# Performance work log

Measured on AMD Instinct MI355X. Metric: run time of the kernel, lower is better.

Reference implementation:

```python
import jax, jax.numpy as jnp
import numpy as np

B, D, H = 16384, 64, 256

def setup_inputs() -> dict:
    key = jax.random.key(0)
    ks = jax.random.split(key, 24)
    s = 0.05
    inp = {
        'x':   jax.random.normal(ks[0], (B, D), dtype=jnp.float32),
        # stacked per-feature MLPs (torch ModuleList of Linear(1,H)->ReLU->Linear(H,H)->ReLU->Linear(H,1))
        'W1':  jax.random.normal(ks[1], (D, H), dtype=jnp.float32) * s,      # in=1
        'b1':  jax.random.normal(ks[2], (D, H), dtype=jnp.float32) * s,
        'W2':  jax.random.normal(ks[3], (D, H, H), dtype=jnp.float32) * s,
        'b2':  jax.random.normal(ks[4], (D, H), dtype=jnp.float32) * s,
        'W3':  jax.random.normal(ks[5], (D, H), dtype=jnp.float32) * s,      # out=1
        'b3':  jax.random.normal(ks[6], (D,), dtype=jnp.float32) * s,
        # attention fusion
        'Wq':  jax.random.normal(ks[7], (H, D), dtype=jnp.float32) * s,
        'bq':  jax.random.normal(ks[8], (H,), dtype=jnp.float32) * s,
        'Wk':  jax.random.normal(ks[9], (H, D), dtype=jnp.float32) * s,
        'bk':  jax.random.normal(ks[10], (H,), dtype=jnp.float32) * s,
        'Ws':  jax.random.normal(ks[11], (D, H), dtype=jnp.float32) * s,
        'bs':  jax.random.normal(ks[12], (D,), dtype=jnp.float32) * s,
        # cross MLP: Linear(D,H)->ReLU->Linear(H,1)
        'Wc1': jax.random.normal(ks[13], (H, D), dtype=jnp.float32) * s,
        'bc1': jax.random.normal(ks[14], (H,), dtype=jnp.float32) * s,
        'Wc2': jax.random.normal(ks[15], (H,), dtype=jnp.float32) * s,
        'bc2': jax.random.normal(ks[16], (1,), dtype=jnp.float32) * s,
        # g_func: Linear(1,H)->ReLU->Linear(H,1)
        'Wg1': jax.random.normal(ks[17], (H,), dtype=jnp.float32) * s,
        'bg1': jax.random.normal(ks[18], (H,), dtype=jnp.float32) * s,
        'Wg2': jax.random.normal(ks[19], (H,), dtype=jnp.float32) * s,
        'bg2': jax.random.normal(ks[20], (1,), dtype=jnp.float32) * s,
    }
    return inp

def reference(x, W1, b1, W2, b2, W3, b3, Wq, bq, Wk, bk, Ws, bs,
              Wc1, bc1, Wc2, bc2, Wg1, bg1, Wg2, bg2):
    # per-feature 3-layer MLPs, vectorized over the feature axis d
    a1 = jax.nn.relu(x[:, :, None] * W1[None] + b1[None])           # [B, D, H]
    a2 = jax.nn.relu(jnp.einsum('bdh,dhk->bdk', a1, W2) + b2[None]) # [B, D, H]
    h_cat = jnp.einsum('bdh,dh->bd', a2, W3) + b3[None]             # [B, D]
    # tiny tanh-softmax attention fusion
    q = h_cat @ Wq.T + bq                                           # [B, H]
    k = h_cat @ Wk.T + bk                                           # [B, H]
    scores = jnp.tanh(q * k) @ Ws.T + bs                            # [B, D]
    wts = jax.nn.softmax(scores, axis=1)
    weighted = jnp.sum(h_cat * wts, axis=1, keepdims=True)          # [B, 1]
    cross = jax.nn.relu(h_cat @ Wc1.T + bc1) @ Wc2[:, None] + bc2   # [B, 1]
    comb = weighted + cross                                         # [B, 1]
    out = jax.nn.relu(comb * Wg1[None] + bg1[None]) @ Wg2[:, None] + bg2  # [B, 1]
    return out
```

## Files before the change

kernel.cpp:

```cpp
#include <hip/hip_runtime.h>
#include <stdint.h>

#define Bn 16384
#define Dn 64
#define Hn 256

typedef short bf16x8 __attribute__((ext_vector_type(8)));
typedef float f32x4 __attribute__((ext_vector_type(4)));
typedef float f32x16 __attribute__((ext_vector_type(16)));

__device__ __forceinline__ unsigned f2bf1(float f) {
  unsigned u = __float_as_uint(f);
  return (u + 0x7FFFu + ((u >> 16) & 1u)) >> 16;
}

__global__ __launch_bounds__(256) void pack_w2(const float* __restrict__ W2,
                                               unsigned short* __restrict__ Bp) {
  int gidx = blockIdx.x * 4 + (threadIdx.x >> 6);
  int lane = threadIdx.x & 63;
  int d  = gidx >> 7;
  int s  = (gidx >> 3) & 15;
  int nb = gidx & 7;
  int k0 = s * 16 + ((lane >> 5) << 3);
  int n  = (nb << 5) + (lane & 31);
  const float* src = W2 + ((size_t)d * Hn + k0) * Hn + n;
  unsigned t[8];
  #pragma unroll
  for (int b = 0; b < 8; ++b) t[b] = f2bf1(src[(size_t)b * Hn]);
  uint4 w;
  w.x = t[0] | (t[1] << 16);
  w.y = t[2] | (t[3] << 16);
  w.z = t[4] | (t[5] << 16);
  w.w = t[6] | (t[7] << 16);
  size_t off = (((size_t)gidx) * 64 + lane) * 8;
  *(uint4*)(Bp + off) = w;
}

__global__ __launch_bounds__(256) void prep_t(
    const float* __restrict__ Wq, const float* __restrict__ Wk,
    const float* __restrict__ Wc1, const float* __restrict__ Ws,
    float* __restrict__ WqT, float* __restrict__ WkT,
    float* __restrict__ Wc1T, float* __restrict__ WsT) {
  int t = blockIdx.x * 256 + threadIdx.x;
  int h = t >> 6, dd = t & 63;
  WqT[dd * 256 + h]  = Wq[h * 64 + dd];
  WkT[dd * 256 + h]  = Wk[h * 64 + dd];
  Wc1T[dd * 256 + h] = Wc1[h * 64 + dd];
  WsT[h * 64 + dd]   = Ws[dd * 256 + h];
}

__global__ __launch_bounds__(768, 1) void gemm_hcat(
    const float* __restrict__ x, const float* __restrict__ W1,
    const float* __restrict__ b1, const float* __restrict__ b2,
    const float* __restrict__ W3, const float* __restrict__ b3,
    const unsigned short* __restrict__ Bp, float* __restrict__ hcT) {
  __shared__ char Bs[131072];

  int bid = blockIdx.x;
  int xcd = bid & 7;
  int dl = (bid >> 3) & 7;
  int chunk = bid >> 6;
  int d = xcd * 8 + dl;
  int base = chunk * 4096;

  int tid = threadIdx.x;
  int lane = tid & 63;
  int w = tid >> 6;
  int l31 = lane & 31;
  int hsel = lane >> 5;

  const unsigned short* BpD = Bp + (size_t)d * 65536;
  const float* W1d = W1 + d * Hn;
  const float* b1d = b1 + d * Hn;
  const float* b2d = b2 + d * Hn;
  const float* W3d = W3 + d * Hn;
  float b3d = b3[d];

  #pragma unroll
  for (int i = 0; i < 11; ++i) {
    int idx = i * 768 + tid;
    if (idx < 8192) {
      const void* g = (const void*)(BpD + (size_t)idx * 8);
      void* l = (void*)(Bs + (size_t)idx * 16);
      __builtin_amdgcn_global_load_lds((const __attribute__((address_space(1))) void*)g,
                                       (__attribute__((address_space(3))) void*)l, 16, 0, 0);
    }
  }
  __syncthreads();

  for (int t = w; t < 128; t += 12) {
    int row = base + t * 32 + l31;
    float xv = x[(size_t)row * Dn + d];

    bf16x8 af[16];
    #pragma unroll
    for (int s = 0; s < 16; ++s) {
      int k = s * 16 + (hsel << 3);
      float4 wa = *(const float4*)(W1d + k);
      float4 wb = *(const float4*)(W1d + k + 4);
      float4 ba = *(const float4*)(b1d + k);
      float4 bb = *(const float4*)(b1d + k + 4);
      float v0 = fmaxf(fmaf(xv, wa.x, ba.x), 0.f);
      float v1 = fmaxf(fmaf(xv, wa.y, ba.y), 0.f);
      float v2 = fmaxf(fmaf(xv, wa.z, ba.z), 0.f);
      float v3 = fmaxf(fmaf(xv, wa.w, ba.w), 0.f);
      float v4 = fmaxf(fmaf(xv, wb.x, bb.x), 0.f);
      float v5 = fmaxf(fmaf(xv, wb.y, bb.y), 0.f);
      float v6 = fmaxf(fmaf(xv, wb.z, bb.z), 0.f);
      float v7 = fmaxf(fmaf(xv, wb.w, bb.w), 0.f);
      union { uint4 u; bf16x8 v; } pk;
      asm("v_cvt_pk_bf16_f32 %0, %1, %2" : "=v"(pk.u.x) : "v"(v0), "v"(v1));
      asm("v_cvt_pk_bf16_f32 %0, %1, %2" : "=v"(pk.u.y) : "v"(v2), "v"(v3));
      asm("v_cvt_pk_bf16_f32 %0, %1, %2" : "=v"(pk.u.z) : "v"(v4), "v"(v5));
      asm("v_cvt_pk_bf16_f32 %0, %1, %2" : "=v"(pk.u.w) : "v"(v6), "v"(v7));
      af[s] = pk.v;
    }

    float ph = 0.f;
    #pragma unroll 1
    for (int nb = 0; nb < 8; ++nb) {
      int cb = (nb << 5) + (hsel << 2);

      f32x16 acc;
      #pragma unroll
      for (int q = 0; q < 4; ++q) {
        float4 bv = *(const float4*)(b2d + cb + (q << 3));
        acc[4 * q + 0] = bv.x;
        acc[4 * q + 1] = bv.y;
        acc[4 * q + 2] = bv.z;
        acc[4 * q + 3] = bv.w;
      }

      __builtin_amdgcn_s_setprio(1);
      #pragma unroll
      for (int s = 0; s < 16; ++s) {
        bf16x8 bfr = *(const bf16x8*)(Bs + ((((s << 3) + nb) << 6) + lane) * 16);
        acc = __builtin_amdgcn_mfma_f32_32x32x16_bf16(bfr, af[s], acc, 0, 0, 0);
      }
      __builtin_amdgcn_s_setprio(0);

      #pragma unroll
      for (int q = 0; q < 4; ++q) {
        float4 wv = *(const float4*)(W3d + cb + (q << 3));
        ph = fmaf(fmaxf(acc[4 * q + 0], 0.f), wv.x, ph);
        ph = fmaf(fmaxf(acc[4 * q + 1], 0.f), wv.y, ph);
        ph = fmaf(fmaxf(acc[4 * q + 2], 0.f), wv.z, ph);
        ph = fmaf(fmaxf(acc[4 * q + 3], 0.f), wv.w, ph);
      }
    }

    ph += __shfl_xor(ph, 32);
    if (lane < 32) hcT[(size_t)d * Bn + row] = ph + b3d;
  }
}

__global__ __launch_bounds__(256) void fused_tail(
    const float* __restrict__ hcT, const float* __restrict__ WqT,
    const float* __restrict__ bq, const float* __restrict__ WkT,
    const float* __restrict__ bk, const float* __restrict__ WsT,
    const float* __restrict__ bs, const float* __restrict__ Wc1T,
    const float* __restrict__ bc1, const float* __restrict__ Wc2,
    const float* __restrict__ bc2, const float* __restrict__ Wg1,
    const float* __restrict__ bg1, const float* __restrict__ Wg2,
    const float* __restrict__ bg2, float* __restrict__ out) {
  __shared__ float hcs[4][4][64];
  __shared__ float ts[4][4][256];
  int wid = threadIdx.x >> 6;
  int lane = threadIdx.x & 63;
  int r0 = (blockIdx.x * 4 + wid) * 4;
  float4 hc4 = *(const float4*)(hcT + (size_t)lane * Bn + r0);
  hcs[wid][0][lane] = hc4.x;
  hcs[wid][1][lane] = hc4.y;
  hcs[wid][2][lane] = hc4.z;
  hcs[wid][3][lane] = hc4.w;
  __syncthreads();

  float qv[4][4], kv[4][4], cv[4][4];
  #pragma unroll
  for (int j = 0; j < 4; ++j) {
    int h = lane + 64 * j;
    float bqv = bq[h], bkv = bk[h], bcv = bc1[h];
    #pragma unroll
    for (int r = 0; r < 4; ++r) { qv[r][j] = bqv; kv[r][j] = bkv; cv[r][j] = bcv; }
  }
  for (int d2 = 0; d2 < 64; ++d2) {
    float hv0 = hcs[wid][0][d2], hv1 = hcs[wid][1][d2];
    float hv2 = hcs[wid][2][d2], hv3 = hcs[wid][3][d2];
    #pragma unroll
    for (int j = 0; j < 4; ++j) {
      int h = lane + 64 * j;
      float wq = WqT[d2 * 256 + h], wk = WkT[d2 * 256 + h], wc = Wc1T[d2 * 256 + h];
      qv[0][j] = fmaf(wq, hv0, qv[0][j]); qv[1][j] = fmaf(wq, hv1, qv[1][j]);
      qv[2][j] = fmaf(wq, hv2, qv[2][j]); qv[3][j] = fmaf(wq, hv3, qv[3][j]);
      kv[0][j] = fmaf(wk, hv0, kv[0][j]); kv[1][j] = fmaf(wk, hv1, kv[1][j]);
      kv[2][j] = fmaf(wk, hv2, kv[2][j]); kv[3][j] = fmaf(wk, hv3, kv[3][j]);
      cv[0][j] = fmaf(wc, hv0, cv[0][j]); cv[1][j] = fmaf(wc, hv1, cv[1][j]);
      cv[2][j] = fmaf(wc, hv2, cv[2][j]); cv[3][j] = fmaf(wc, hv3, cv[3][j]);
    }
  }
  #pragma unroll
  for (int r = 0; r < 4; ++r)
    #pragma unroll
    for (int j = 0; j < 4; ++j)
      ts[wid][r][lane + 64 * j] = tanhf(qv[r][j] * kv[r][j]);
  __syncthreads();

  float sc[4];
  { float b = bs[lane]; sc[0] = b; sc[1] = b; sc[2] = b; sc[3] = b; }
  for (int h2 = 0; h2 < 256; ++h2) {
    float w = WsT[h2 * 64 + lane];
    sc[0] = fmaf(w, ts[wid][0][h2], sc[0]);
    sc[1] = fmaf(w, ts[wid][1][h2], sc[1]);
    sc[2] = fmaf(w, ts[wid][2][h2], sc[2]);
    sc[3] = fmaf(w, ts[wid][3][h2], sc[3]);
  }

  float hcr[4] = {hc4.x, hc4.y, hc4.z, hc4.w};
  float res[4];
  #pragma unroll
  for (int r = 0; r < 4; ++r) {
    float s = sc[r];
    float mx = s;
    #pragma unroll
    for (int off = 1; off < 64; off <<= 1) mx = fmaxf(mx, __shfl_xor(mx, off));
    float e = __expf(s - mx);
    float se = e;
    #pragma unroll
    for (int off = 1; off < 64; off <<= 1) se += __shfl_xor(se, off);
    float wgt = hcr[r] * (e / se);
    #pragma unroll
    for (int off = 1; off < 64; off <<= 1) wgt += __shfl_xor(wgt, off);
    float cp = 0.f;
    #pragma unroll
    for (int j = 0; j < 4; ++j) cp = fmaf(fmaxf(cv[r][j], 0.f), Wc2[lane + 64 * j], cp);
    #pragma unroll
    for (int off = 1; off < 64; off <<= 1) cp += __shfl_xor(cp, off);
    float comb = wgt + cp + bc2[0];
    float fp = 0.f;
    #pragma unroll
    for (int j = 0; j < 4; ++j) {
      int h = lane + 64 * j;
      fp = fmaf(fmaxf(fmaf(comb, Wg1[h], bg1[h]), 0.f), Wg2[h], fp);
    }
    #pragma unroll
    for (int off = 1; off < 64; off <<= 1) fp += __shfl_xor(fp, off);
    res[r] = fp + bg2[0];
  }
  if (lane == 0) {
    float4 o = make_float4(res[0], res[1], res[2], res[3]);
    *(float4*)(out + r0) = o;
  }
}

extern "C" void kernel_launch(void* const* d_in, const int* in_sizes, int n_in,
                              void* d_out, int out_size, void* d_ws, size_t ws_size,
                              hipStream_t stream) {
  const float* x   = (const float*)d_in[0];
  const float* W1  = (const float*)d_in[1];
  const float* b1  = (const float*)d_in[2];
  const float* W2  = (const float*)d_in[3];
  const float* b2  = (const float*)d_in[4];
  const float* W3  = (const float*)d_in[5];
  const float* b3  = (const float*)d_in[6];
  const float* Wq  = (const float*)d_in[7];
  const float* bq  = (const float*)d_in[8];
  const float* Wk  = (const float*)d_in[9];
  const float* bk  = (const float*)d_in[10];
  const float* Ws  = (const float*)d_in[11];
  const float* bs  = (const float*)d_in[12];
  const float* Wc1 = (const float*)d_in[13];
  const float* bc1 = (const float*)d_in[14];
  const float* Wc2 = (const float*)d_in[15];
  const float* bc2 = (const float*)d_in[16];
  const float* Wg1 = (const float*)d_in[17];
  const float* bg1 = (const float*)d_in[18];
  const float* Wg2 = (const float*)d_in[19];
  const float* bg2 = (const float*)d_in[20];

  unsigned short* Bp = (unsigned short*)d_ws;
  float* hcT  = (float*)((char*)d_ws + 8388608);
  float* WqT  = (float*)((char*)d_ws + 12582912);
  float* WkT  = WqT + 16384;
  float* Wc1T = WkT + 16384;
  float* WsT  = Wc1T + 16384;

  pack_w2<<<2048, 256, 0, stream>>>(W2, Bp);
  prep_t<<<64, 256, 0, stream>>>(Wq, Wk, Wc1, Ws, WqT, WkT, Wc1T, WsT);
  gemm_hcat<<<256, 768, 0, stream>>>(x, W1, b1, b2, W3, b3, Bp, hcT);
  fused_tail<<<1024, 256, 0, stream>>>(hcT, WqT, bq, WkT, bk, WsT, bs, Wc1T, bc1,
                                       Wc2, bc2, Wg1, bg1, Wg2, bg2, (float*)d_out);
}
```

Measured before the change: 204.1 us.

## Register-block four row tiles per wave to reuse LDS B fragments across MFMAs

Each wave now processes four 32-row tiles at once, so every bf16 W2 fragment read from LDS feeds four MFMAs instead of one. This cuts LDS read traffic per MFMA and gives four independent accumulator chains. The block drops from 12 to 8 waves so the 128 tiles split evenly, and the first-layer activation math uses packed float2 ops. The cost is far more registers: four A-fragment sets and four accumulators, which risks spilling, with fewer waves available to hide latency.

```diff
diff --git a/kernel.cpp b/kernel.cpp
--- a/kernel.cpp
+++ b/kernel.cpp
@@ -6,6 +6,7 @@
 #define Hn 256
 
 typedef short bf16x8 __attribute__((ext_vector_type(8)));
+typedef float f32x2 __attribute__((ext_vector_type(2)));
 typedef float f32x4 __attribute__((ext_vector_type(4)));
 typedef float f32x16 __attribute__((ext_vector_type(16)));
 
@@ -49,7 +50,7 @@
   WsT[h * 64 + dd]   = Ws[dd * 256 + h];
 }
 
-__global__ __launch_bounds__(768, 1) void gemm_hcat(
+__global__ __launch_bounds__(512, 1) void gemm_hcat(
     const float* __restrict__ x, const float* __restrict__ W1,
     const float* __restrict__ b1, const float* __restrict__ b2,
     const float* __restrict__ W3, const float* __restrict__ b3,
@@ -77,80 +78,97 @@
   float b3d = b3[d];
 
   #pragma unroll
-  for (int i = 0; i < 11; ++i) {
-    int idx = i * 768 + tid;
-    if (idx < 8192) {
-      const void* g = (const void*)(BpD + (size_t)idx * 8);
-      void* l = (void*)(Bs + (size_t)idx * 16);
-      __builtin_amdgcn_global_load_lds((const __attribute__((address_space(1))) void*)g,
-                                       (__attribute__((address_space(3))) void*)l, 16, 0, 0);
-    }
+  for (int i = 0; i < 16; ++i) {
+    int idx = i * 512 + tid;
+    const void* g = (const void*)(BpD + (size_t)idx * 8);
+    void* l = (void*)(Bs + (size_t)idx * 16);
+    __builtin_amdgcn_global_load_lds((const __attribute__((address_space(1))) void*)g,
+                                     (__attribute__((address_space(3))) void*)l, 16, 0, 0);
   }
   __syncthreads();
 
-  for (int t = w; t < 128; t += 12) {
-    int row = base + t * 32 + l31;
-    float xv = x[(size_t)row * Dn + d];
-
-    bf16x8 af[16];
+  for (int p = 0; p < 4; ++p) {
+    int t0 = w * 16 + p * 4;
+    int row[4];
+    float xv[4];
+    #pragma unroll
+    for (int j = 0; j < 4; ++j) {
+      row[j] = base + (t0 + j) * 32 + l31;
+      xv[j] = x[(size_t)row[j] * Dn + d];
+    }
+
+    bf16x8 af[4][16];
     #pragma unroll
     for (int s = 0; s < 16; ++s) {
       int k = s * 16 + (hsel << 3);
-      float4 wa = *(const float4*)(W1d + k);
-      float4 wb = *(const float4*)(W1d + k + 4);
-      float4 ba = *(const float4*)(b1d + k);
-      float4 bb = *(const float4*)(b1d + k + 4);
-      float v0 = fmaxf(fmaf(xv, wa.x, ba.x), 0.f);
-      float v1 = fmaxf(fmaf(xv, wa.y, ba.y), 0.f);
-      float v2 = fmaxf(fmaf(xv, wa.z, ba.z), 0.f);
-      float v3 = fmaxf(fmaf(xv, wa.w, ba.w), 0.f);
-      float v4 = fmaxf(fmaf(xv, wb.x, bb.x), 0.f);
-      float v5 = fmaxf(fmaf(xv, wb.y, bb.y), 0.f);
-      float v6 = fmaxf(fmaf(xv, wb.z, bb.z), 0.f);
-      float v7 = fmaxf(fmaf(xv, wb.w, bb.w), 0.f);
-      union { uint4 u; bf16x8 v; } pk;
-      asm("v_cvt_pk_bf16_f32 %0, %1, %2" : "=v"(pk.u.x) : "v"(v0), "v"(v1));
-      asm("v_cvt_pk_bf16_f32 %0, %1, %2" : "=v"(pk.u.y) : "v"(v2), "v"(v3));
-      asm("v_cvt_pk_bf16_f32 %0, %1, %2" : "=v"(pk.u.z) : "v"(v4), "v"(v5));
-      asm("v_cvt_pk_bf16_f32 %0, %1, %2" : "=v"(pk.u.w) : "v"(v6), "v"(v7));
-      af[s] = pk.v;
-    }
-
-    float ph = 0.f;
+      const f32x2* w1p = (const f32x2*)(W1d + k);
+      const f32x2* b1p = (const f32x2*)(b1d + k);
+      f32x2 wv0 = w1p[0], wv1 = w1p[1], wv2 = w1p[2], wv3 = w1p[3];
+      f32x2 bv0 = b1p[0], bv1 = b1p[1], bv2 = b1p[2], bv3 = b1p[3];
+      f32x2 z = {0.f, 0.f};
+      #pragma unroll
+      for (int j = 0; j < 4; ++j) {
+        f32x2 xr = {xv[j], xv[j]};
+        f32x2 p0 = __builtin_elementwise_max(xr * wv0 + bv0, z);
+        f32x2 p1 = __builtin_elementwise_max(xr * wv1 + bv1, z);
+        f32x2 p2 = __builtin_elementwise_max(xr * wv2 + bv2, z);
+        f32x2 p3 = __builtin_elementwise_max(xr * wv3 + bv3, z);
+        union { uint4 u; bf16x8 v; } pk;
+        asm("v_cvt_pk_bf16_f32 %0, %1, %2" : "=v"(pk.u.x) : "v"(p0.x), "v"(p0.y));
+        asm("v_cvt_pk_bf16_f32 %0, %1, %2" : "=v"(pk.u.y) : "v"(p1.x), "v"(p1.y));
+        asm("v_cvt_pk_bf16_f32 %0, %1, %2" : "=v"(pk.u.z) : "v"(p2.x), "v"(p2.y));
+        asm("v_cvt_pk_bf16_f32 %0, %1, %2" : "=v"(pk.u.w) : "v"(p3.x), "v"(p3.y));
+        af[j][s] = pk.v;
+      }
+    }
+
+    float ph[4] = {0.f, 0.f, 0.f, 0.f};
     #pragma unroll 1
     for (int nb = 0; nb < 8; ++nb) {
       int cb = (nb << 5) + (hsel << 2);
 
-      f32x16 acc;
+      f32x16 acc[4];
       #pragma unroll
       for (int q = 0; q < 4; ++q) {
         float4 bv = *(const float4*)(b2d + cb + (q << 3));
-        acc[4 * q + 0] = bv.x;
-        acc[4 * q + 1] = bv.y;
-        acc[4 * q + 2] = bv.z;
-        acc[4 * q + 3] = bv.w;
+        #pragma unroll
+        for (int j = 0; j < 4; ++j) {
+          acc[j][4 * q + 0] = bv.x;
+          acc[j][4 * q + 1] = bv.y;
+          acc[j][4 * q + 2] = bv.z;
+          acc[j][4 * q + 3] = bv.w;
+        }
       }
 
       __builtin_amdgcn_s_setprio(1);
       #pragma unroll
       for (int s = 0; s < 16; ++s) {
         bf16x8 bfr = *(const bf16x8*)(Bs + ((((s << 3) + nb) << 6) + lane) * 16);
-        acc = __builtin_amdgcn_mfma_f32_32x32x16_bf16(bfr, af[s], acc, 0, 0, 0);
+        acc[0] = __builtin_amdgcn_mfma_f32_32x32x16_bf16(bfr, af[0][s], acc[0], 0, 0, 0);
+        acc[1] = __builtin_amdgcn_mfma_f32_32x32x16_bf16(bfr, af[1][s], acc[1], 0, 0, 0);
+        acc[2] = __builtin_amdgcn_mfma_f32_32x32x16_bf16(bfr, af[2][s], acc[2], 0, 0, 0);
+        acc[3] = __builtin_amdgcn_mfma_f32_32x32x16_bf16(bfr, af[3][s], acc[3], 0, 0, 0);
       }
       __builtin_amdgcn_s_setprio(0);
 
       #pragma unroll
       for (int q = 0; q < 4; ++q) {
         float4 wv = *(const float4*)(W3d + cb + (q << 3));
-        ph = fmaf(fmaxf(acc[4 * q + 0], 0.f), wv.x, ph);
-        ph = fmaf(fmaxf(acc[4 * q + 1], 0.f), wv.y, ph);
-        ph = fmaf(fmaxf(acc[4 * q + 2], 0.f), wv.z, ph);
-        ph = fmaf(fmaxf(acc[4 * q + 3], 0.f), wv.w, ph);
+        #pragma unroll
+        for (int j = 0; j < 4; ++j) {
+          ph[j] = fmaf(fmaxf(acc[j][4 * q + 0], 0.f), wv.x, ph[j]);
+          ph[j] = fmaf(fmaxf(acc[j][4 * q + 1], 0.f), wv.y, ph[j]);
+          ph[j] = fmaf(fmaxf(acc[j][4 * q + 2], 0.f), wv.z, ph[j]);
+          ph[j] = fmaf(fmaxf(acc[j][4 * q + 3], 0.f), wv.w, ph[j]);
+        }
       }
     }
 
-    ph += __shfl_xor(ph, 32);
-    if (lane < 32) hcT[(size_t)d * Bn + row] = ph + b3d;
+    #pragma unroll
+    for (int j = 0; j < 4; ++j) {
+      ph[j] += __shfl_xor(ph[j], 32);
+      if (lane < 32) hcT[(size_t)d * Bn + row[j]] = ph[j] + b3d;
+    }
   }
 }
 
@@ -286,7 +304,7 @@
 
   pack_w2<<<2048, 256, 0, stream>>>(W2, Bp);
   prep_t<<<64, 256, 0, stream>>>(Wq, Wk, Wc1, Ws, WqT, WkT, Wc1T, WsT);
-  gemm_hcat<<<256, 768, 0, stream>>>(x, W1, b1, b2, W3, b3, Bp, hcT);
+  gemm_hcat<<<256, 512, 0, stream>>>(x, W1, b1, b2, W3, b3, Bp, hcT);
   fused_tail<<<1024, 256, 0, stream>>>(hcT, WqT, bq, WkT, bk, WsT, bs, Wc1T, bc1,
                                        Wc2, bc2, Wg1, bg1, Wg2, bg2, (float*)d_out);
 }
```

Result: slower. 426.9 us (+109.2%).
